# Kernel optimization log

Hardware: AMD Instinct MI355X
Metric: run time of the kernel (lower is better)

The kernel has to match this reference:

```python
import jax, jax.numpy as jnp
import numpy as np
import math

N_EMBD = 1024
N_HEAD = 16
HEAD_DIM = N_EMBD // N_HEAD
# Faithful to source: scores = QK^T / scale, where scale = 1/sqrt(head_dim)
# => scores = QK^T * sqrt(head_dim)
INV_SCALE = math.sqrt(HEAD_DIM)


def setup_inputs() -> dict:
    key = jax.random.key(0)
    ks = jax.random.split(key, 9)
    B, S = 4, 2048
    x = jax.random.normal(ks[0], (B, S, N_EMBD), dtype=jnp.float32)
    init = 1.0 / math.sqrt(N_EMBD)
    def lin(kw, kb):
        W = jax.random.uniform(kw, (N_EMBD, N_EMBD), jnp.float32, -init, init)
        b = jax.random.uniform(kb, (N_EMBD,), jnp.float32, -init, init)
        return W, b
    Wq, bq = lin(ks[1], ks[2])
    Wk, bk = lin(ks[3], ks[4])
    Wv, bv = lin(ks[5], ks[6])
    Wo, bo = lin(ks[7], ks[8])
    return {"x": x, "Wq": Wq, "bq": bq, "Wk": Wk, "bk": bk,
            "Wv": Wv, "bv": bv, "Wo": Wo, "bo": bo}


def reference(x, Wq, bq, Wk, bk, Wv, bv, Wo, bo):
    B, S, _ = x.shape
    # projections (torch Linear: y = x @ W^T + b; here weights stored [in,out])
    q = (x @ Wq + bq).reshape(B, S, N_HEAD, HEAD_DIM)
    k = (x @ Wk + bk).reshape(B, S, N_HEAD, HEAD_DIM)
    v = (x @ Wv + bv).reshape(B, S, N_HEAD, HEAD_DIM)
    # scores: [B, H, S, S]; note unusual scaling (divide by 1/sqrt(d))
    scores = jnp.einsum('bqhd,bkhd->bhqk', q, k) * INV_SCALE
    attn = jax.nn.softmax(scores, axis=-1)
    # dropout in eval mode -> identity
    out = jnp.einsum('bhqk,bkhd->bqhd', attn, v).reshape(B, S, N_EMBD)
    return out @ Wo + bo
```

## Files before the change

kernel.cpp:

```cpp
#include <hip/hip_runtime.h>
#include <hip/hip_bf16.h>

#define DEVI static __device__ __forceinline__

typedef __attribute__((ext_vector_type(8))) _Float16 f16x8;
typedef __attribute__((ext_vector_type(4))) float f32x4;
typedef __attribute__((ext_vector_type(8))) unsigned short u16x8;
typedef unsigned short u16;

constexpr int NE = 1024;
constexpr int NH = 16;
constexpr int HD = 64;
constexpr int SB = 4;
constexpr int SS = 2048;
constexpr int MR = SB * SS;

DEVI u16 f2h(float f) {
  union { _Float16 h; u16 u; } x;
  x.h = (_Float16)f;
  return x.u;
}

DEVI void gload_lds16(const void* g, void* l) {
  __builtin_amdgcn_global_load_lds(
      (const __attribute__((address_space(1))) unsigned int*)g,
      (__attribute__((address_space(3))) unsigned int*)l, 16, 0, 0);
}

__global__ void k_cvt_x(const float* __restrict__ x, u16* __restrict__ xb) {
  size_t i = (size_t)blockIdx.x * 256 + threadIdx.x;
  const f32x4* s4 = (const f32x4*)x;
  f32x4 a = s4[2 * i], c = s4[2 * i + 1];
  u16x8 o;
  o[0] = f2h(a[0]); o[1] = f2h(a[1]); o[2] = f2h(a[2]); o[3] = f2h(a[3]);
  o[4] = f2h(c[0]); o[5] = f2h(c[1]); o[6] = f2h(c[2]); o[7] = f2h(c[3]);
  ((u16x8*)xb)[i] = o;
}

__global__ void k_wt(const float* __restrict__ W0, const float* __restrict__ W1,
                     const float* __restrict__ W2, const float* __restrict__ W3,
                     u16* __restrict__ WT) {
  __shared__ float tile[64][65];
  const float* W = (blockIdx.z == 0) ? W0 : (blockIdx.z == 1) ? W1 : (blockIdx.z == 2) ? W2 : W3;
  u16* T = WT + (size_t)blockIdx.z * NE * NE;
  int tid = threadIdx.x, c = tid & 63, rr = tid >> 6;
  int ti = blockIdx.y * 64, tj = blockIdx.x * 64;
#pragma unroll
  for (int p = 0; p < 16; p++) {
    int r = p * 4 + rr;
    tile[r][c] = W[(size_t)(ti + r) * NE + tj + c];
  }
  __syncthreads();
#pragma unroll
  for (int p = 0; p < 16; p++) {
    int r = p * 4 + rr;
    T[(size_t)(tj + r) * NE + ti + c] = f2h(tile[c][r]);
  }
}

template <int MODE>
__global__ __launch_bounds__(256) void k_gemm(const u16* __restrict__ A,
                                              const u16* __restrict__ BT,
                                              const float* __restrict__ bias,
                                              void* __restrict__ outp) {
  __shared__ __align__(16) u16 lA[128 * 64];
  __shared__ __align__(16) u16 lB[128 * 64];
  const int tid = threadIdx.x;
  const int wave = tid >> 6, lane = tid & 63;
  const int wr = wave >> 1, wc = wave & 1;
  const int fr = lane & 15, fg = lane >> 4;
  const int srow = lane >> 3;
  const int scol = ((lane & 7) ^ srow) * 8;
  const int mb = blockIdx.x, nb = blockIdx.y;
  f32x4 acc[4][4] = {};
  for (int kt = 0; kt < NE / 64; ++kt) {
#pragma unroll
    for (int p = 0; p < 4; p++) {
      int rb = wave * 32 + p * 8;
      gload_lds16(A + (size_t)(mb * 128 + rb + srow) * NE + kt * 64 + scol, lA + rb * 64);
      gload_lds16(BT + (size_t)(nb * 128 + rb + srow) * NE + kt * 64 + scol, lB + rb * 64);
    }
    __syncthreads();
#pragma unroll
    for (int kd = 0; kd < 2; ++kd) {
      f16x8 af[4], bg[4];
#pragma unroll
      for (int mi = 0; mi < 4; mi++) {
        int row = wr * 64 + mi * 16 + fr;
        af[mi] = *(const f16x8*)((const char*)lA + row * 128 + ((kd * 64 + fg * 16) ^ ((row & 7) << 4)));
      }
#pragma unroll
      for (int nj = 0; nj < 4; nj++) {
        int row = wc * 64 + nj * 16 + fr;
        bg[nj] = *(const f16x8*)((const char*)lB + row * 128 + ((kd * 64 + fg * 16) ^ ((row & 7) << 4)));
      }
#pragma unroll
      for (int mi = 0; mi < 4; mi++)
#pragma unroll
        for (int nj = 0; nj < 4; nj++)
          acc[mi][nj] = __builtin_amdgcn_mfma_f32_16x16x32_f16(af[mi], bg[nj], acc[mi][nj], 0, 0, 0);
    }
    __syncthreads();
  }
  float bv[4];
#pragma unroll
  for (int nj = 0; nj < 4; nj++) bv[nj] = bias[nb * 128 + wc * 64 + nj * 16 + fr];
#pragma unroll
  for (int mi = 0; mi < 4; mi++)
#pragma unroll
    for (int nj = 0; nj < 4; nj++)
#pragma unroll
      for (int r = 0; r < 4; r++) {
        int row = mb * 128 + wr * 64 + mi * 16 + fg * 4 + r;
        int col = nb * 128 + wc * 64 + nj * 16 + fr;
        float v = acc[mi][nj][r] + bv[nj];
        if constexpr (MODE == 2) {
          ((float*)outp)[(size_t)row * NE + col] = v;
        } else if constexpr (MODE == 0) {
          ((u16*)outp)[(size_t)row * NE + col] = f2h(v);
        } else {
          int b = row >> 11, s = row & (SS - 1);
          int h = col >> 6, d = col & 63;
          ((u16*)outp)[(((size_t)(b * NH + h) * HD + d) << 11) | (size_t)s] = f2h(v);
        }
      }
}

__global__ __launch_bounds__(256) void k_attn(const u16* __restrict__ Q, const u16* __restrict__ K,
                                              const u16* __restrict__ VT, u16* __restrict__ AO) {
  __shared__ __align__(16) u16 lK[2][64 * 64];
  __shared__ __align__(16) u16 lV[2][64 * 64];
  __shared__ __align__(16) u16 lP[4][32 * 72];
  const int tid = threadIdx.x, wave = tid >> 6, lane = tid & 63;
  const int fr = lane & 15, fg = lane >> 4;
  const int srow = lane >> 3;
  const int scol = ((lane & 7) ^ srow) * 8;
  const int qb = blockIdx.x * 128, h = blockIdx.y, b = blockIdx.z;
  const u16* Kg = K + (size_t)(b * SS) * NE + h * HD;
  const u16* Vg = VT + (size_t)(b * NH + h) * HD * SS;
  f16x8 qf[2][2];
#pragma unroll
  for (int g = 0; g < 2; g++) {
    const u16* Qp = Q + (size_t)(b * SS + qb + wave * 32 + g * 16 + fr) * NE + h * HD;
    qf[g][0] = *(const f16x8*)(Qp + fg * 8);
    qf[g][1] = *(const f16x8*)(Qp + 32 + fg * 8);
  }
  f32x4 acc[2][4] = {};
  float m_s[2] = {-1e30f, -1e30f}, l_s[2] = {0.f, 0.f};
  const float SC = 8.0f * 1.44269504088896340736f;
  u16* Pw = &lP[wave][0];

  auto STAGE = [&](int kt2, int bufi) {
    u16* lk = &lK[bufi][0];
    u16* lv = &lV[bufi][0];
#pragma unroll
    for (int p = 0; p < 2; p++) {
      int rb = wave * 16 + p * 8;
      gload_lds16(Kg + (size_t)(kt2 * 64 + rb + srow) * NE + scol, lk + rb * 64);
      gload_lds16(Vg + (size_t)(rb + srow) * SS + kt2 * 64 + scol, lv + rb * 64);
    }
  };

  STAGE(0, 0);
  for (int kt = 0; kt < SS / 64; ++kt) {
    const int cur = kt & 1;
    __syncthreads();
    if (kt + 1 < SS / 64) STAGE(kt + 1, cur ^ 1);
    const u16* lk = &lK[cur][0];
    const u16* lv = &lV[cur][0];
#pragma unroll
    for (int g = 0; g < 2; g++) {
      f32x4 st[4];
#pragma unroll
      for (int c = 0; c < 4; c++) {
        f32x4 z = {};
#pragma unroll
        for (int kd = 0; kd < 2; ++kd) {
          int row = c * 16 + fr;
          f16x8 kf = *(const f16x8*)((const char*)lk + row * 128 + ((kd * 64 + fg * 16) ^ ((row & 7) << 4)));
          z = __builtin_amdgcn_mfma_f32_16x16x32_f16(kf, qf[g][kd], z, 0, 0, 0);
        }
        st[c] = z;
      }
      float rmax = fmaxf(fmaxf(fmaxf(st[0][0], st[0][1]), fmaxf(st[0][2], st[0][3])),
                         fmaxf(fmaxf(st[1][0], st[1][1]), fmaxf(st[1][2], st[1][3])));
      float rm2  = fmaxf(fmaxf(fmaxf(st[2][0], st[2][1]), fmaxf(st[2][2], st[2][3])),
                         fmaxf(fmaxf(st[3][0], st[3][1]), fmaxf(st[3][2], st[3][3])));
      rmax = fmaxf(rmax, rm2) * SC;
      rmax = fmaxf(rmax, __shfl_xor(rmax, 16));
      rmax = fmaxf(rmax, __shfl_xor(rmax, 32));
      float mo = m_s[g];
      float mu = mo;
      if (!__all(rmax <= mo + 8.f)) {
        float nm = fmaxf(mo, rmax);
        float fs = __builtin_amdgcn_exp2f(mo - nm);
        m_s[g] = nm; mu = nm;
        l_s[g] *= fs;
#pragma unroll
        for (int c2 = 0; c2 < 4; c2++)
#pragma unroll
          for (int r = 0; r < 4; r++) acc[g][c2][r] *= fs;
      }
      float rs = 0.f;
#pragma unroll
      for (int c = 0; c < 4; c++) {
        union { _Float16 h[4]; unsigned long long u; } pk;
#pragma unroll
        for (int r = 0; r < 4; r++) {
          float p = __builtin_amdgcn_exp2f(st[c][r] * SC - mu);
          rs += p;
          pk.h[r] = (_Float16)p;
        }
        *(unsigned long long*)((char*)Pw + (g * 16 + fr) * 144 + c * 32 + fg * 8) = pk.u;
      }
      rs += __shfl_xor(rs, 16);
      rs += __shfl_xor(rs, 32);
      l_s[g] += rs;
      f16x8 pf[2];
#pragma unroll
      for (int ks = 0; ks < 2; ks++)
        pf[ks] = *(const f16x8*)((const char*)Pw + (g * 16 + fr) * 144 + ks * 64 + fg * 16);
#pragma unroll
      for (int c2 = 0; c2 < 4; c2++)
#pragma unroll
        for (int ks = 0; ks < 2; ks++) {
          int row = c2 * 16 + fr;
          f16x8 vf = *(const f16x8*)((const char*)lv + row * 128 + ((ks * 64 + fg * 16) ^ ((row & 7) << 4)));
          acc[g][c2] = __builtin_amdgcn_mfma_f32_16x16x32_f16(vf, pf[ks], acc[g][c2], 0, 0, 0);
        }
    }
  }
#pragma unroll
  for (int g = 0; g < 2; g++) {
    float inv = 1.0f / l_s[g];
    u16* dst = AO + (size_t)(b * SS + qb + wave * 32 + g * 16 + fr) * NE + h * HD;
#pragma unroll
    for (int c2 = 0; c2 < 4; c2++) {
      union { _Float16 h[4]; unsigned long long u; } o;
#pragma unroll
      for (int r = 0; r < 4; r++) o.h[r] = (_Float16)(acc[g][c2][r] * inv);
      *(unsigned long long*)(dst + c2 * 16 + fg * 4) = o.u;
    }
  }
}

extern "C" void kernel_launch(void* const* d_in, const int* in_sizes, int n_in,
                              void* d_out, int out_size, void* d_ws, size_t ws_size,
                              hipStream_t stream) {
  const float* x  = (const float*)d_in[0];
  const float* Wq = (const float*)d_in[1]; const float* bq = (const float*)d_in[2];
  const float* Wk = (const float*)d_in[3]; const float* bk = (const float*)d_in[4];
  const float* Wv = (const float*)d_in[5]; const float* bv = (const float*)d_in[6];
  const float* Wo = (const float*)d_in[7]; const float* bo = (const float*)d_in[8];

  u16* xb  = (u16*)d_ws;
  u16* WT  = xb  + (size_t)MR * NE;
  u16* Qb  = WT  + (size_t)4 * NE * NE;
  u16* Kb  = Qb  + (size_t)MR * NE;
  u16* VTb = Kb  + (size_t)MR * NE;
  u16* AOb = xb;

  k_cvt_x<<<dim3(MR * NE / (256 * 8)), 256, 0, stream>>>(x, xb);
  k_wt<<<dim3(16, 16, 4), 256, 0, stream>>>(Wq, Wk, Wv, Wo, WT);

  dim3 gg(MR / 128, NE / 128);
  k_gemm<0><<<gg, 256, 0, stream>>>(xb, WT + 0 * (size_t)NE * NE, bq, Qb);
  k_gemm<0><<<gg, 256, 0, stream>>>(xb, WT + 1 * (size_t)NE * NE, bk, Kb);
  k_gemm<1><<<gg, 256, 0, stream>>>(xb, WT + 2 * (size_t)NE * NE, bv, VTb);

  k_attn<<<dim3(SS / 128, NH, SB), 256, 0, stream>>>(Qb, Kb, VTb, AOb);

  k_gemm<2><<<gg, 256, 0, stream>>>(AOb, WT + 3 * (size_t)NE * NE, bo, (float*)d_out);
}
```

Baseline: 240.5 us.

## Switch attention to 32x32x16 MFMA with register-resident P via lane shuffles

Rewrites the attention inner loop so that QK^T and PV use 32x32x16 MFMA tiles instead of 16x16x32. The P matrix is packed with cvt_pkrtz and redistributed between half-waves using shuffles, so it no longer makes a round trip through LDS. Each lane now owns one query row, which simplifies the row max and sum reductions and drops the second g loop. The output epilogue stages results through LDS so each row is written to global memory as one coalesced 16-byte vector. The risks are higher register pressure from the f32x16 accumulators and the p[2][16] array, and rounding changes from round-toward-zero packing.

```diff
diff --git a/kernel.cpp b/kernel.cpp
--- a/kernel.cpp
+++ b/kernel.cpp
@@ -4,8 +4,11 @@
 #define DEVI static __device__ __forceinline__
 
 typedef __attribute__((ext_vector_type(8))) _Float16 f16x8;
+typedef __attribute__((ext_vector_type(2))) __fp16 fp16v2;
 typedef __attribute__((ext_vector_type(4))) float f32x4;
+typedef __attribute__((ext_vector_type(16))) float f32x16;
 typedef __attribute__((ext_vector_type(8))) unsigned short u16x8;
+typedef __attribute__((ext_vector_type(4))) unsigned int u32x4;
 typedef unsigned short u16;
 
 constexpr int NE = 1024;
@@ -19,6 +22,12 @@
   union { _Float16 h; u16 u; } x;
   x.h = (_Float16)f;
   return x.u;
+}
+
+DEVI unsigned pk2(float lo, float hi) {
+  union { fp16v2 h2; unsigned u; } cv;
+  cv.h2 = __builtin_amdgcn_cvt_pkrtz(lo, hi);
+  return cv.u;
 }
 
 DEVI void gload_lds16(const void* g, void* l) {
@@ -128,31 +137,25 @@
 
 __global__ __launch_bounds__(256) void k_attn(const u16* __restrict__ Q, const u16* __restrict__ K,
                                               const u16* __restrict__ VT, u16* __restrict__ AO) {
-  __shared__ __align__(16) u16 lK[2][64 * 64];
-  __shared__ __align__(16) u16 lV[2][64 * 64];
-  __shared__ __align__(16) u16 lP[4][32 * 72];
+  __shared__ __align__(16) u16 smem[4 * 4096];
   const int tid = threadIdx.x, wave = tid >> 6, lane = tid & 63;
-  const int fr = lane & 15, fg = lane >> 4;
+  const int q32 = lane & 31, hh = lane >> 5;
   const int srow = lane >> 3;
   const int scol = ((lane & 7) ^ srow) * 8;
   const int qb = blockIdx.x * 128, h = blockIdx.y, b = blockIdx.z;
   const u16* Kg = K + (size_t)(b * SS) * NE + h * HD;
   const u16* Vg = VT + (size_t)(b * NH + h) * HD * SS;
-  f16x8 qf[2][2];
-#pragma unroll
-  for (int g = 0; g < 2; g++) {
-    const u16* Qp = Q + (size_t)(b * SS + qb + wave * 32 + g * 16 + fr) * NE + h * HD;
-    qf[g][0] = *(const f16x8*)(Qp + fg * 8);
-    qf[g][1] = *(const f16x8*)(Qp + 32 + fg * 8);
-  }
-  f32x4 acc[2][4] = {};
-  float m_s[2] = {-1e30f, -1e30f}, l_s[2] = {0.f, 0.f};
+  const u16* Qp = Q + (size_t)(b * SS + qb + wave * 32 + q32) * NE + h * HD;
+  f16x8 qf[4];
+#pragma unroll
+  for (int m = 0; m < 4; m++) qf[m] = *(const f16x8*)(Qp + m * 16 + hh * 8);
+  f32x16 oacc[2] = {};
+  float m_s = -1e30f, l_s = 0.f;
   const float SC = 8.0f * 1.44269504088896340736f;
-  u16* Pw = &lP[wave][0];
 
   auto STAGE = [&](int kt2, int bufi) {
-    u16* lk = &lK[bufi][0];
-    u16* lv = &lV[bufi][0];
+    u16* lk = smem + bufi * 4096;
+    u16* lv = smem + 8192 + bufi * 4096;
 #pragma unroll
     for (int p = 0; p < 2; p++) {
       int rb = wave * 16 + p * 8;
@@ -166,81 +169,111 @@
     const int cur = kt & 1;
     __syncthreads();
     if (kt + 1 < SS / 64) STAGE(kt + 1, cur ^ 1);
-    const u16* lk = &lK[cur][0];
-    const u16* lv = &lV[cur][0];
-#pragma unroll
-    for (int g = 0; g < 2; g++) {
-      f32x4 st[4];
-#pragma unroll
-      for (int c = 0; c < 4; c++) {
-        f32x4 z = {};
-#pragma unroll
-        for (int kd = 0; kd < 2; ++kd) {
-          int row = c * 16 + fr;
-          f16x8 kf = *(const f16x8*)((const char*)lk + row * 128 + ((kd * 64 + fg * 16) ^ ((row & 7) << 4)));
-          z = __builtin_amdgcn_mfma_f32_16x16x32_f16(kf, qf[g][kd], z, 0, 0, 0);
+    const u16* lk = smem + cur * 4096;
+    const u16* lv = smem + 8192 + cur * 4096;
+    f32x16 sacc[2];
+#pragma unroll
+    for (int kt32 = 0; kt32 < 2; kt32++) {
+      f32x16 z = {};
+      int row = kt32 * 32 + q32;
+#pragma unroll
+      for (int m = 0; m < 4; m++) {
+        f16x8 kf = *(const f16x8*)((const char*)lk + row * 128 + ((m * 32 + hh * 16) ^ ((row & 7) << 4)));
+        z = __builtin_amdgcn_mfma_f32_32x32x16_f16(kf, qf[m], z, 0, 0, 0);
+      }
+      sacc[kt32] = z;
+    }
+    float mx = sacc[0][0];
+#pragma unroll
+    for (int r = 1; r < 16; r++) mx = fmaxf(mx, sacc[0][r]);
+#pragma unroll
+    for (int r = 0; r < 16; r++) mx = fmaxf(mx, sacc[1][r]);
+    mx *= SC;
+    mx = fmaxf(mx, __shfl_xor(mx, 32));
+    float mo = m_s, mu = mo;
+    if (!__all(mx <= mo + 8.f)) {
+      float nm = fmaxf(mo, mx);
+      float fs = __builtin_amdgcn_exp2f(mo - nm);
+      m_s = nm; mu = nm; l_s *= fs;
+#pragma unroll
+      for (int d2 = 0; d2 < 2; d2++)
+#pragma unroll
+        for (int r = 0; r < 16; r++) oacc[d2][r] *= fs;
+    }
+    float rs = 0.f;
+    float p[2][16];
+#pragma unroll
+    for (int kt32 = 0; kt32 < 2; kt32++)
+#pragma unroll
+      for (int r = 0; r < 16; r++) {
+        float pv = __builtin_amdgcn_exp2f(sacc[kt32][r] * SC - mu);
+        p[kt32][r] = pv;
+        rs += pv;
+      }
+    rs += __shfl_xor(rs, 32);
+    l_s += rs;
+    unsigned W[2][4][2];
+#pragma unroll
+    for (int kt32 = 0; kt32 < 2; kt32++)
+#pragma unroll
+      for (int a = 0; a < 4; a++)
+#pragma unroll
+        for (int b2 = 0; b2 < 2; b2++)
+          W[kt32][a][b2] = pk2(p[kt32][4 * a + 2 * b2], p[kt32][4 * a + 2 * b2 + 1]);
+    unsigned bw[4][4];
+#pragma unroll
+    for (int kt32 = 0; kt32 < 2; kt32++)
+#pragma unroll
+      for (int tau = 0; tau < 2; tau++)
+#pragma unroll
+        for (int b2 = 0; b2 < 2; b2++) {
+          unsigned Y = W[kt32][2 * tau][b2];
+          unsigned X = W[kt32][2 * tau + 1][b2];
+          unsigned sx = __shfl_xor(X, 32);
+          unsigned sy = __shfl_xor(Y, 32);
+          int t = kt32 * 2 + tau;
+          bw[t][b2]     = hh ? sx : Y;
+          bw[t][b2 + 2] = hh ? X : sy;
         }
-        st[c] = z;
-      }
-      float rmax = fmaxf(fmaxf(fmaxf(st[0][0], st[0][1]), fmaxf(st[0][2], st[0][3])),
-                         fmaxf(fmaxf(st[1][0], st[1][1]), fmaxf(st[1][2], st[1][3])));
-      float rm2  = fmaxf(fmaxf(fmaxf(st[2][0], st[2][1]), fmaxf(st[2][2], st[2][3])),
-                         fmaxf(fmaxf(st[3][0], st[3][1]), fmaxf(st[3][2], st[3][3])));
-      rmax = fmaxf(rmax, rm2) * SC;
-      rmax = fmaxf(rmax, __shfl_xor(rmax, 16));
-      rmax = fmaxf(rmax, __shfl_xor(rmax, 32));
-      float mo = m_s[g];
-      float mu = mo;
-      if (!__all(rmax <= mo + 8.f)) {
-        float nm = fmaxf(mo, rmax);
-        float fs = __builtin_amdgcn_exp2f(mo - nm);
-        m_s[g] = nm; mu = nm;
-        l_s[g] *= fs;
-#pragma unroll
-        for (int c2 = 0; c2 < 4; c2++)
-#pragma unroll
-          for (int r = 0; r < 4; r++) acc[g][c2][r] *= fs;
-      }
-      float rs = 0.f;
-#pragma unroll
-      for (int c = 0; c < 4; c++) {
-        union { _Float16 h[4]; unsigned long long u; } pk;
-#pragma unroll
-        for (int r = 0; r < 4; r++) {
-          float p = __builtin_amdgcn_exp2f(st[c][r] * SC - mu);
-          rs += p;
-          pk.h[r] = (_Float16)p;
-        }
-        *(unsigned long long*)((char*)Pw + (g * 16 + fr) * 144 + c * 32 + fg * 8) = pk.u;
-      }
-      rs += __shfl_xor(rs, 16);
-      rs += __shfl_xor(rs, 32);
-      l_s[g] += rs;
-      f16x8 pf[2];
-#pragma unroll
-      for (int ks = 0; ks < 2; ks++)
-        pf[ks] = *(const f16x8*)((const char*)Pw + (g * 16 + fr) * 144 + ks * 64 + fg * 16);
-#pragma unroll
-      for (int c2 = 0; c2 < 4; c2++)
-#pragma unroll
-        for (int ks = 0; ks < 2; ks++) {
-          int row = c2 * 16 + fr;
-          f16x8 vf = *(const f16x8*)((const char*)lv + row * 128 + ((ks * 64 + fg * 16) ^ ((row & 7) << 4)));
-          acc[g][c2] = __builtin_amdgcn_mfma_f32_16x16x32_f16(vf, pf[ks], acc[g][c2], 0, 0, 0);
-        }
-    }
-  }
-#pragma unroll
-  for (int g = 0; g < 2; g++) {
-    float inv = 1.0f / l_s[g];
-    u16* dst = AO + (size_t)(b * SS + qb + wave * 32 + g * 16 + fr) * NE + h * HD;
-#pragma unroll
-    for (int c2 = 0; c2 < 4; c2++) {
-      union { _Float16 h[4]; unsigned long long u; } o;
-#pragma unroll
-      for (int r = 0; r < 4; r++) o.h[r] = (_Float16)(acc[g][c2][r] * inv);
-      *(unsigned long long*)(dst + c2 * 16 + fg * 4) = o.u;
-    }
+    f16x8 pf[4];
+#pragma unroll
+    for (int t = 0; t < 4; t++) {
+      union { unsigned w[4]; f16x8 v; } u;
+#pragma unroll
+      for (int w = 0; w < 4; w++) u.w[w] = bw[t][w];
+      pf[t] = u.v;
+    }
+#pragma unroll
+    for (int d2 = 0; d2 < 2; d2++) {
+      int row = d2 * 32 + q32;
+#pragma unroll
+      for (int t = 0; t < 4; t++) {
+        f16x8 vf = *(const f16x8*)((const char*)lv + row * 128 + ((t * 32 + hh * 16) ^ ((row & 7) << 4)));
+        oacc[d2] = __builtin_amdgcn_mfma_f32_32x32x16_f16(vf, pf[t], oacc[d2], 0, 0, 0);
+      }
+    }
+  }
+  __syncthreads();
+  unsigned* epi = (unsigned*)smem + wave * (32 * 36);
+  float inv = 1.0f / l_s;
+#pragma unroll
+  for (int d2 = 0; d2 < 2; d2++)
+#pragma unroll
+    for (int a = 0; a < 4; a++)
+#pragma unroll
+      for (int b2 = 0; b2 < 2; b2++) {
+        int r0 = 4 * a + 2 * b2;
+        epi[q32 * 36 + d2 * 16 + 4 * a + 2 * hh + b2] =
+            pk2(oacc[d2][r0] * inv, oacc[d2][r0 + 1] * inv);
+      }
+  __syncthreads();
+  {
+    int q2 = lane >> 1, part = lane & 1;
+    const unsigned* src = (const unsigned*)smem + wave * (32 * 36) + q2 * 36 + part * 16;
+    u16* dst = AO + (size_t)(b * SS + qb + wave * 32 + q2) * NE + h * HD + part * 32;
+#pragma unroll
+    for (int u = 0; u < 4; u++)
+      *(u32x4*)(dst + u * 8) = *(const u32x4*)(src + u * 4);
   }
 }
 
```

Result: faster. 225.3 us (-6.3%).
